# Performance work log

Measured on AMD Instinct MI355X. Metric: run time of the kernel, lower is better.

Reference implementation:

```python
import jax, jax.numpy as jnp
import numpy as np

N = 524288          # query points
N_COMP = 36         # sdf_n_comp
GRID = 512          # cubic grid resolution
SDF_DIM = 256
APP_DIM = 128
MAT_MODE = [(0, 1), (0, 2), (1, 2)]
VEC_MODE = [2, 1, 0]
PE_FREQS = (1.0, 2.0, 4.0)  # sdf_multires=3, log-sampled 2^0..2^2


def _pos_enc(x):
    # NeRF embedder, include_input=True: [x, sin(f x), cos(f x) per freq]
    outs = [x]
    for f in PE_FREQS:
        outs.append(jnp.sin(x * f))
        outs.append(jnp.cos(x * f))
    return jnp.concatenate(outs, axis=-1)  # (N, 21)


def _bilinear_plane(plane, gx, gy):
    # plane: (C, H, W); gx indexes W, gy indexes H; align_corners=True
    C, H, W = plane.shape
    px = (gx + 1.0) * 0.5 * (W - 1)
    py = (gy + 1.0) * 0.5 * (H - 1)
    x0 = jnp.clip(jnp.floor(px), 0, W - 2).astype(jnp.int32)
    y0 = jnp.clip(jnp.floor(py), 0, H - 2).astype(jnp.int32)
    x1, y1 = x0 + 1, y0 + 1
    wx = px - x0
    wy = py - y0
    f00 = plane[:, y0, x0]  # (C, N)
    f01 = plane[:, y0, x1]
    f10 = plane[:, y1, x0]
    f11 = plane[:, y1, x1]
    return (f00 * (1 - wx) + f01 * wx) * (1 - wy) + (f10 * (1 - wx) + f11 * wx) * wy


def _linear_line(line, g):
    # line: (C, L); g in [-1, 1]; align_corners=True
    C, L = line.shape
    p = (g + 1.0) * 0.5 * (L - 1)
    i0 = jnp.clip(jnp.floor(p), 0, L - 2).astype(jnp.int32)
    w = p - i0
    return line[:, i0] * (1 - w) + line[:, i0 + 1] * w  # (C, N)


def setup_inputs() -> dict:
    key = jax.random.key(0)
    ks = jax.random.split(key, 6)
    xyz = jax.random.uniform(ks[0], (N, 3), dtype=jnp.float32)  # points in aabb [0,1]^3
    planes = jax.random.normal(ks[1], (3, N_COMP, GRID, GRID), dtype=jnp.float32) * 0.1
    lines = jax.random.normal(ks[2], (3, N_COMP, GRID), dtype=jnp.float32) * 0.1
    in_ch = N_COMP * 3 + 21  # 129
    W1 = jax.random.normal(ks[3], (in_ch, SDF_DIM), dtype=jnp.float32) * (np.sqrt(2.0) / np.sqrt(SDF_DIM))
    b1 = jnp.zeros((SDF_DIM,), dtype=jnp.float32)
    W2 = jax.random.normal(ks[4], (SDF_DIM, 1 + APP_DIM), dtype=jnp.float32) * 0.0001 + np.sqrt(np.pi) / np.sqrt(SDF_DIM)
    b2 = jnp.full((1 + APP_DIM,), -0.2, dtype=jnp.float32)  # init_radius bias
    return {"xyz": xyz, "planes": planes, "lines": lines, "W1": W1, "b1": b1, "W2": W2, "b2": b2}


def reference(xyz, planes, lines, W1, b1, W2, b2):
    # contraction: normalize aabb [0,1]^3 -> [-1,1]
    xn = 2.0 * xyz - 1.0  # (N, 3)
    # sampling coords are detached in the original (coordinate_plane.detach())
    xs = jax.lax.stop_gradient(xn)
    feats = []
    for i in range(3):
        m0, m1 = MAT_MODE[i]
        pfeat = _bilinear_plane(planes[i], xs[:, m0], xs[:, m1])  # (C, N)
        lfeat = _linear_line(lines[i], xs[:, VEC_MODE[i]])        # (C, N)
        feats.append(pfeat * lfeat)
    feat = jnp.concatenate(feats, axis=0).T  # (N, 3C)
    pe = _pos_enc(xn)                         # (N, 21)
    h = jnp.concatenate([feat, pe], axis=-1)  # (N, 129)
    h = jax.nn.softplus(100.0 * (h @ W1 + b1)) / 100.0  # Softplus(beta=100)
    out = h @ W2 + b2  # (N, 1 + app_dim); out[..., :1] is the SDF
    return out
```

## Files before the change

### kernel.cpp

```cpp
#include <hip/hip_runtime.h>
#include <math.h>

typedef unsigned short u16;
typedef unsigned int u32;
typedef __attribute__((ext_vector_type(2))) u32 u32x2;
typedef __attribute__((ext_vector_type(8))) short short8;
typedef __attribute__((ext_vector_type(4))) float f32x4;

#define OFF_LINES_T 62914560u
#define OFF_W1S     63037440u
#define OFF_W2S     63119360u
#define WS_NEEDED   63217664u

__device__ __forceinline__ float bf_lo(u32 u){ union{u32 i;float f;} v; v.i = u << 16; return v.f; }
__device__ __forceinline__ float bf_hi(u32 u){ union{u32 i;float f;} v; v.i = u & 0xffff0000u; return v.f; }
__device__ __forceinline__ u16 f2bf(float f){ union{float f;u32 i;} v; v.f=f; u32 i=v.i; return (u16)((i + 0x7fffu + ((i>>16)&1u)) >> 16); }
__device__ __forceinline__ u32 pack2bf(float lo, float hi){ return (u32)f2bf(lo) | ((u32)f2bf(hi)<<16); }
__device__ __forceinline__ u32 pack2bf_fast(float lo, float hi){
  return __builtin_amdgcn_perm(__float_as_uint(hi) + 0x8000u,
                               __float_as_uint(lo) + 0x8000u, 0x07060302u);
}
__device__ __forceinline__ u16 f2bf_fast(float f){ return (u16)((__float_as_uint(f) + 0x8000u) >> 16); }

__global__ void k_tp(const float* __restrict__ planes, u16* __restrict__ pt){
  int t = blockIdx.x*256 + threadIdx.x;
  int i = t >> 18;
  int yx = t & 262143;
  const float* src = planes + (size_t)i*9437184 + yx;
  uint4* dst = reinterpret_cast<uint4*>(pt + (size_t)t*40);
#pragma unroll
  for (int cc=0; cc<5; cc++){
    float v[8];
#pragma unroll
    for (int e=0;e<8;e++){
      int c = cc*8+e;
      v[e] = (c<36) ? src[(size_t)c*262144] : 0.f;
    }
    uint4 o; o.x=pack2bf(v[0],v[1]); o.y=pack2bf(v[2],v[3]); o.z=pack2bf(v[4],v[5]); o.w=pack2bf(v[6],v[7]);
    dst[cc]=o;
  }
}

__global__ void k_tl(const float* __restrict__ lines, u16* __restrict__ lt){
  int t = blockIdx.x*256 + threadIdx.x;
  int i = t >> 9, g = t & 511;
  const float* src = lines + (size_t)i*18432 + g;
  uint4* dst = reinterpret_cast<uint4*>(lt + (size_t)t*40);
#pragma unroll
  for (int cc=0; cc<5; cc++){
    float v[8];
#pragma unroll
    for (int e=0;e<8;e++){
      int c = cc*8+e;
      v[e] = (c<36) ? src[(size_t)c*512] : 0.f;
    }
    uint4 o; o.x=pack2bf(v[0],v[1]); o.y=pack2bf(v[2],v[3]); o.z=pack2bf(v[4],v[5]); o.w=pack2bf(v[6],v[7]);
    dst[cc]=o;
  }
}

__device__ __forceinline__ int map_k1(int kp){
  if (kp < 120){ int g = kp/40, r = kp - g*40; return (r<36) ? g*36 + r : -1; }
  if (kp < 141) return kp - 12;
  return -1;
}

__global__ void k_w1(const float* __restrict__ W1, u16* __restrict__ w1s){
  int t = blockIdx.x*256 + threadIdx.x;
  int lane = t & 63;
  int fid = t >> 6;
  int nt = fid/5, kt = fid - nt*5;
  int n = nt*16 + (lane & 15);
  int kb = kt*32 + (lane >> 4)*8;
  float v[8];
#pragma unroll
  for (int j=0;j<8;j++){ int k = map_k1(kb+j); v[j] = (k>=0) ? W1[k*256+n] : 0.f; }
  uint4 o; o.x=pack2bf(v[0],v[1]); o.y=pack2bf(v[2],v[3]); o.z=pack2bf(v[4],v[5]); o.w=pack2bf(v[6],v[7]);
  *reinterpret_cast<uint4*>(w1s + (size_t)t*8) = o;
}

__global__ void k_w2(const float* __restrict__ W2, u16* __restrict__ w2s){
  int t = blockIdx.x*256 + threadIdx.x;
  int lane = t & 63;
  int fid = t >> 6;
  int kb = (fid & 7)*32 + (lane >> 4)*8;
  int n = (fid >> 3)*16 + (lane & 15);
  float v[8];
#pragma unroll
  for (int j=0;j<8;j++){ int k = kb+j; v[j] = (n<129) ? W2[k*129+n] : 0.f; }
  uint4 o; o.x=pack2bf(v[0],v[1]); o.y=pack2bf(v[2],v[3]); o.z=pack2bf(v[4],v[5]); o.w=pack2bf(v[6],v[7]);
  *reinterpret_cast<uint4*>(w2s + (size_t)t*8) = o;
}

__device__ __forceinline__ u32 blend(u32 u00,u32 u01,u32 u10,u32 u11,u32 g0,u32 g1,
                                     float wx,float wy,float wz){
  float r[2];
#pragma unroll
  for (int h=0; h<2; h++){
    float f00 = h ? bf_hi(u00) : bf_lo(u00);
    float f01 = h ? bf_hi(u01) : bf_lo(u01);
    float f10 = h ? bf_hi(u10) : bf_lo(u10);
    float f11 = h ? bf_hi(u11) : bf_lo(u11);
    float e0  = h ? bf_hi(g0)  : bf_lo(g0);
    float e1  = h ? bf_hi(g1)  : bf_lo(g1);
    float a  = f00 + (f01-f00)*wx;
    float b  = f10 + (f11-f10)*wx;
    float pf = a + (b-a)*wy;
    float lf = e0 + (e1-e0)*wz;
    r[h] = pf*lf;
  }
  return pack2bf_fast(r[0], r[1]);
}

#define FSTRIDE 168
#define HSTRIDE 264

__global__ void __launch_bounds__(512, 4) k_main(
    const float* __restrict__ xyz, const u16* __restrict__ pt,
    const u16* __restrict__ lt, const u16* __restrict__ w1s,
    const u16* __restrict__ w2s, const float* __restrict__ b1,
    const float* __restrict__ b2, float* __restrict__ out)
{
  __shared__ u16 smem[64*HSTRIDE];
  const int tid = threadIdx.x;
  const int p = tid >> 3, q = tid & 7;
  const int gp = blockIdx.x*64 + p;
  const float u0 = xyz[gp*3], u1 = xyz[gp*3+1], u2 = xyz[gp*3+2];
  const float xn0 = 2.f*u0-1.f, xn1 = 2.f*u1-1.f, xn2 = 2.f*u2-1.f;

  if (q < 6){
    const int i = q >> 1, part = q & 1;
    float gxv, gyv, gzv;
    if      (i==0){ gxv=xn0; gyv=xn1; gzv=xn2; }
    else if (i==1){ gxv=xn0; gyv=xn2; gzv=xn1; }
    else          { gxv=xn1; gyv=xn2; gzv=xn0; }
    float px=(gxv+1.0f)*0.5f*511.0f, py=(gyv+1.0f)*0.5f*511.0f, pz=(gzv+1.0f)*0.5f*511.0f;
    float fx=fminf(fmaxf(floorf(px),0.f),510.f);
    float fy=fminf(fmaxf(floorf(py),0.f),510.f);
    float fz=fminf(fmaxf(floorf(pz),0.f),510.f);
    int ix=(int)fx, iy=(int)fy, iz=(int)fz;
    float wx=px-fx, wy=py-fy, wz=pz-fz;
    const u16* base  = pt + (size_t)((i<<18)+(iy<<9)+ix)*40 + part*20;
    const u16* lbase = lt + (size_t)((i<<9)+iz)*40 + part*20;
    u16* dst = smem + p*FSTRIDE + i*40 + part*20;
#pragma unroll
    for (int c=0; c<5; c++){
      u32x2 a00 = *reinterpret_cast<const u32x2*>(base + c*4);
      u32x2 a01 = *reinterpret_cast<const u32x2*>(base + 40 + c*4);
      u32x2 a10 = *reinterpret_cast<const u32x2*>(base + 20480 + c*4);
      u32x2 a11 = *reinterpret_cast<const u32x2*>(base + 20520 + c*4);
      u32x2 e0  = *reinterpret_cast<const u32x2*>(lbase + c*4);
      u32x2 e1  = *reinterpret_cast<const u32x2*>(lbase + 40 + c*4);
      u32x2 o;
      o.x = blend(a00.x,a01.x,a10.x,a11.x,e0.x,e1.x,wx,wy,wz);
      o.y = blend(a00.y,a01.y,a10.y,a11.y,e0.y,e1.y,wx,wy,wz);
      *reinterpret_cast<u32x2*>(dst + c*4) = o;
    }
  } else if (q == 6){
    float v[21];
    v[0]=xn0; v[1]=xn1; v[2]=xn2;
    v[3]=__sinf(xn0);      v[4]=__sinf(xn1);      v[5]=__sinf(xn2);
    v[6]=__cosf(xn0);      v[7]=__cosf(xn1);      v[8]=__cosf(xn2);
    v[9]=__sinf(2.f*xn0);  v[10]=__sinf(2.f*xn1); v[11]=__sinf(2.f*xn2);
    v[12]=__cosf(2.f*xn0); v[13]=__cosf(2.f*xn1); v[14]=__cosf(2.f*xn2);
    v[15]=__sinf(4.f*xn0); v[16]=__sinf(4.f*xn1); v[17]=__sinf(4.f*xn2);
    v[18]=__cosf(4.f*xn0); v[19]=__cosf(4.f*xn1); v[20]=__cosf(4.f*xn2);
    u16* dst = smem + p*FSTRIDE + 120;
#pragma unroll
    for (int c=0; c<20; c++){
      float a = (c*2  <21)?v[c*2  ]:0.f;
      float b = (c*2+1<21)?v[c*2+1]:0.f;
      *reinterpret_cast<u32*>(dst + c*2) = pack2bf_fast(a,b);
    }
  }
  __syncthreads();

  const int lane = tid & 63;
  const int w = tid >> 6;
  const int wm = w & 1, wn = w >> 1;
  const int lm = lane & 15;
  const int quad = lane >> 4;
  const f32x4 zero = {0.f,0.f,0.f,0.f};
  f32x4 acc1[2][4];
#pragma unroll
  for (int mt=0; mt<2; mt++)
#pragma unroll
    for (int nt=0; nt<4; nt++) acc1[mt][nt] = zero;

#pragma unroll
  for (int kt=0; kt<5; kt++){
    short8 a[2];
#pragma unroll
    for (int mt=0; mt<2; mt++)
      a[mt] = *reinterpret_cast<const short8*>(smem + ((wm*2+mt)*16 + lm)*FSTRIDE + kt*32 + quad*8);
    short8 b[4];
#pragma unroll
    for (int nt=0; nt<4; nt++)
      b[nt] = *reinterpret_cast<const short8*>(w1s + (size_t)(((wn*4+nt)*5 + kt)*64 + lane)*8);
#pragma unroll
    for (int mt=0; mt<2; mt++)
#pragma unroll
      for (int nt=0; nt<4; nt++)
        acc1[mt][nt] = __builtin_amdgcn_mfma_f32_16x16x32_bf16(a[mt], b[nt], acc1[mt][nt], 0,0,0);
  }
  __syncthreads();

#pragma unroll
  for (int nt=0; nt<4; nt++){
    int col = wn*64 + nt*16 + lm;
    float bias = b1[col];
#pragma unroll
    for (int mt=0; mt<2; mt++){
#pragma unroll
      for (int r=0; r<4; r++){
        float xv = acc1[mt][nt][r] + bias;
        float z = 100.f*xv;
        float y = (z > 15.f) ? xv : __logf(1.f + __expf(z))*0.01f;
        int row = (wm*2+mt)*16 + quad*4 + r;
        smem[row*HSTRIDE + col] = f2bf_fast(y);
      }
    }
  }
  __syncthreads();

  f32x4 acc2[2][3];
#pragma unroll
  for (int mt=0; mt<2; mt++)
#pragma unroll
    for (int nt=0; nt<3; nt++) acc2[mt][nt] = zero;

#pragma unroll
  for (int kt=0; kt<8; kt++){
    short8 a[2];
#pragma unroll
    for (int mt=0; mt<2; mt++)
      a[mt] = *reinterpret_cast<const short8*>(smem + ((wm*2+mt)*16 + lm)*HSTRIDE + kt*32 + quad*8);
    short8 b[3];
#pragma unroll
    for (int nt=0; nt<3; nt++){
      int ntg = wn*3 + nt;
      b[nt] = *reinterpret_cast<const short8*>(w2s + (size_t)((ntg*8 + kt)*64 + lane)*8);
    }
#pragma unroll
    for (int mt=0; mt<2; mt++)
#pragma unroll
      for (int nt=0; nt<3; nt++)
        acc2[mt][nt] = __builtin_amdgcn_mfma_f32_16x16x32_bf16(a[mt], b[nt], acc2[mt][nt], 0,0,0);
  }

#pragma unroll
  for (int nt=0; nt<3; nt++){
    int j = (wn*3 + nt)*16 + lm;
    if (j < 129){
      float bias = b2[j];
#pragma unroll
      for (int mt=0; mt<2; mt++){
#pragma unroll
        for (int r=0; r<4; r++){
          int row = (wm*2+mt)*16 + quad*4 + r;
          out[(size_t)(blockIdx.x*64 + row)*129 + j] = acc2[mt][nt][r] + bias;
        }
      }
    }
  }
}

extern "C" void kernel_launch(void* const* d_in, const int* in_sizes, int n_in,
                              void* d_out, int out_size, void* d_ws, size_t ws_size,
                              hipStream_t stream) {
  const float* xyz    = (const float*)d_in[0];
  const float* planes = (const float*)d_in[1];
  const float* lines  = (const float*)d_in[2];
  const float* W1     = (const float*)d_in[3];
  const float* b1     = (const float*)d_in[4];
  const float* W2     = (const float*)d_in[5];
  const float* b2     = (const float*)d_in[6];
  if (ws_size < (size_t)WS_NEEDED) return;

  u16* pt  = (u16*)((char*)d_ws);
  u16* lt  = (u16*)((char*)d_ws + OFF_LINES_T);
  u16* w1s = (u16*)((char*)d_ws + OFF_W1S);
  u16* w2s = (u16*)((char*)d_ws + OFF_W2S);

  k_tp<<<3072, 256, 0, stream>>>(planes, pt);
  k_tl<<<6,    256, 0, stream>>>(lines,  lt);
  k_w1<<<20,   256, 0, stream>>>(W1, w1s);
  k_w2<<<24,   256, 0, stream>>>(W2, w2s);
  k_main<<<8192, 512, 0, stream>>>(xyz, pt, lt, w1s, w2s, b1, b2, (float*)d_out);
}
```

Baseline: 657.9 us.

## Merge preprocessing kernels, batch gather loads, packed blend, balance PE work, nontemporal stores

Measured after the change: 673.1 us. +2.3%, slower.

```diff
diff --git a/kernel.cpp b/kernel.cpp
--- a/kernel.cpp
+++ b/kernel.cpp
@@ -6,6 +6,7 @@
 typedef __attribute__((ext_vector_type(2))) u32 u32x2;
 typedef __attribute__((ext_vector_type(8))) short short8;
 typedef __attribute__((ext_vector_type(4))) float f32x4;
+typedef __attribute__((ext_vector_type(2))) float f32x2;
 
 #define OFF_LINES_T 62914560u
 #define OFF_W1S     63037440u
@@ -22,94 +23,95 @@
 }
 __device__ __forceinline__ u16 f2bf_fast(float f){ return (u16)((__float_as_uint(f) + 0x8000u) >> 16); }
 
-__global__ void k_tp(const float* __restrict__ planes, u16* __restrict__ pt){
-  int t = blockIdx.x*256 + threadIdx.x;
-  int i = t >> 18;
-  int yx = t & 262143;
-  const float* src = planes + (size_t)i*9437184 + yx;
-  uint4* dst = reinterpret_cast<uint4*>(pt + (size_t)t*40);
-#pragma unroll
-  for (int cc=0; cc<5; cc++){
-    float v[8];
-#pragma unroll
-    for (int e=0;e<8;e++){
-      int c = cc*8+e;
-      v[e] = (c<36) ? src[(size_t)c*262144] : 0.f;
-    }
-    uint4 o; o.x=pack2bf(v[0],v[1]); o.y=pack2bf(v[2],v[3]); o.z=pack2bf(v[4],v[5]); o.w=pack2bf(v[6],v[7]);
-    dst[cc]=o;
-  }
-}
-
-__global__ void k_tl(const float* __restrict__ lines, u16* __restrict__ lt){
-  int t = blockIdx.x*256 + threadIdx.x;
-  int i = t >> 9, g = t & 511;
-  const float* src = lines + (size_t)i*18432 + g;
-  uint4* dst = reinterpret_cast<uint4*>(lt + (size_t)t*40);
-#pragma unroll
-  for (int cc=0; cc<5; cc++){
-    float v[8];
-#pragma unroll
-    for (int e=0;e<8;e++){
-      int c = cc*8+e;
-      v[e] = (c<36) ? src[(size_t)c*512] : 0.f;
-    }
-    uint4 o; o.x=pack2bf(v[0],v[1]); o.y=pack2bf(v[2],v[3]); o.z=pack2bf(v[4],v[5]); o.w=pack2bf(v[6],v[7]);
-    dst[cc]=o;
-  }
-}
-
 __device__ __forceinline__ int map_k1(int kp){
   if (kp < 120){ int g = kp/40, r = kp - g*40; return (r<36) ? g*36 + r : -1; }
   if (kp < 141) return kp - 12;
   return -1;
 }
 
-__global__ void k_w1(const float* __restrict__ W1, u16* __restrict__ w1s){
-  int t = blockIdx.x*256 + threadIdx.x;
-  int lane = t & 63;
-  int fid = t >> 6;
-  int nt = fid/5, kt = fid - nt*5;
-  int n = nt*16 + (lane & 15);
-  int kb = kt*32 + (lane >> 4)*8;
-  float v[8];
-#pragma unroll
-  for (int j=0;j<8;j++){ int k = map_k1(kb+j); v[j] = (k>=0) ? W1[k*256+n] : 0.f; }
-  uint4 o; o.x=pack2bf(v[0],v[1]); o.y=pack2bf(v[2],v[3]); o.z=pack2bf(v[4],v[5]); o.w=pack2bf(v[6],v[7]);
-  *reinterpret_cast<uint4*>(w1s + (size_t)t*8) = o;
-}
-
-__global__ void k_w2(const float* __restrict__ W2, u16* __restrict__ w2s){
-  int t = blockIdx.x*256 + threadIdx.x;
-  int lane = t & 63;
-  int fid = t >> 6;
-  int kb = (fid & 7)*32 + (lane >> 4)*8;
-  int n = (fid >> 3)*16 + (lane & 15);
-  float v[8];
-#pragma unroll
-  for (int j=0;j<8;j++){ int k = kb+j; v[j] = (n<129) ? W2[k*129+n] : 0.f; }
-  uint4 o; o.x=pack2bf(v[0],v[1]); o.y=pack2bf(v[2],v[3]); o.z=pack2bf(v[4],v[5]); o.w=pack2bf(v[6],v[7]);
-  *reinterpret_cast<uint4*>(w2s + (size_t)t*8) = o;
-}
-
-__device__ __forceinline__ u32 blend(u32 u00,u32 u01,u32 u10,u32 u11,u32 g0,u32 g1,
-                                     float wx,float wy,float wz){
-  float r[2];
-#pragma unroll
-  for (int h=0; h<2; h++){
-    float f00 = h ? bf_hi(u00) : bf_lo(u00);
-    float f01 = h ? bf_hi(u01) : bf_lo(u01);
-    float f10 = h ? bf_hi(u10) : bf_lo(u10);
-    float f11 = h ? bf_hi(u11) : bf_lo(u11);
-    float e0  = h ? bf_hi(g0)  : bf_lo(g0);
-    float e1  = h ? bf_hi(g1)  : bf_lo(g1);
-    float a  = f00 + (f01-f00)*wx;
-    float b  = f10 + (f11-f10)*wx;
-    float pf = a + (b-a)*wy;
-    float lf = e0 + (e1-e0)*wz;
-    r[h] = pf*lf;
-  }
-  return pack2bf_fast(r[0], r[1]);
+#define NB_TP 3072
+#define NB_TL 6
+#define NB_W1 20
+#define NB_W2 24
+__global__ void k_pre(const float* __restrict__ planes, const float* __restrict__ lines,
+                      const float* __restrict__ W1, const float* __restrict__ W2,
+                      u16* __restrict__ pt, u16* __restrict__ lt,
+                      u16* __restrict__ w1s, u16* __restrict__ w2s){
+  const int b = blockIdx.x;
+  const int tid = threadIdx.x;
+  if (b < NB_TP){
+    int t = b*256 + tid;
+    int i = t >> 18;
+    int yx = t & 262143;
+    const float* src = planes + (size_t)i*9437184 + yx;
+    uint4* dst = reinterpret_cast<uint4*>(pt + (size_t)t*40);
+#pragma unroll
+    for (int cc=0; cc<5; cc++){
+      float v[8];
+#pragma unroll
+      for (int e=0;e<8;e++){
+        int c = cc*8+e;
+        v[e] = (c<36) ? src[(size_t)c*262144] : 0.f;
+      }
+      uint4 o; o.x=pack2bf(v[0],v[1]); o.y=pack2bf(v[2],v[3]); o.z=pack2bf(v[4],v[5]); o.w=pack2bf(v[6],v[7]);
+      dst[cc]=o;
+    }
+  } else if (b < NB_TP+NB_TL){
+    int t = (b-NB_TP)*256 + tid;
+    int i = t >> 9, g = t & 511;
+    const float* src = lines + (size_t)i*18432 + g;
+    uint4* dst = reinterpret_cast<uint4*>(lt + (size_t)t*40);
+#pragma unroll
+    for (int cc=0; cc<5; cc++){
+      float v[8];
+#pragma unroll
+      for (int e=0;e<8;e++){
+        int c = cc*8+e;
+        v[e] = (c<36) ? src[(size_t)c*512] : 0.f;
+      }
+      uint4 o; o.x=pack2bf(v[0],v[1]); o.y=pack2bf(v[2],v[3]); o.z=pack2bf(v[4],v[5]); o.w=pack2bf(v[6],v[7]);
+      dst[cc]=o;
+    }
+  } else if (b < NB_TP+NB_TL+NB_W1){
+    int t = (b-(NB_TP+NB_TL))*256 + tid;
+    int lane = t & 63;
+    int fid = t >> 6;
+    int nt = fid/5, kt = fid - nt*5;
+    int n = nt*16 + (lane & 15);
+    int kb = kt*32 + (lane >> 4)*8;
+    float v[8];
+#pragma unroll
+    for (int j=0;j<8;j++){ int k = map_k1(kb+j); v[j] = (k>=0) ? W1[k*256+n] : 0.f; }
+    uint4 o; o.x=pack2bf(v[0],v[1]); o.y=pack2bf(v[2],v[3]); o.z=pack2bf(v[4],v[5]); o.w=pack2bf(v[6],v[7]);
+    *reinterpret_cast<uint4*>(w1s + (size_t)t*8) = o;
+  } else {
+    int t = (b-(NB_TP+NB_TL+NB_W1))*256 + tid;
+    int lane = t & 63;
+    int fid = t >> 6;
+    int kb = (fid & 7)*32 + (lane >> 4)*8;
+    int n = (fid >> 3)*16 + (lane & 15);
+    float v[8];
+#pragma unroll
+    for (int j=0;j<8;j++){ int k = kb+j; v[j] = (n<129) ? W2[k*129+n] : 0.f; }
+    uint4 o; o.x=pack2bf(v[0],v[1]); o.y=pack2bf(v[2],v[3]); o.z=pack2bf(v[4],v[5]); o.w=pack2bf(v[6],v[7]);
+    *reinterpret_cast<uint4*>(w2s + (size_t)t*8) = o;
+  }
+}
+
+__device__ __forceinline__ f32x2 bfx2(u32 u){
+  f32x2 r;
+  r.x = __uint_as_float(u << 16);
+  r.y = __uint_as_float(u & 0xffff0000u);
+  return r;
+}
+
+__device__ __forceinline__ u32 blend2(u32 u00,u32 u01,u32 u10,u32 u11,u32 g0,u32 g1,
+                                      float w00,float w01,float w10,float w11,
+                                      float v0,float v1){
+  f32x2 pf = bfx2(u00)*w00 + bfx2(u01)*w01 + bfx2(u10)*w10 + bfx2(u11)*w11;
+  f32x2 lf = bfx2(g0)*v0 + bfx2(g1)*v1;
+  f32x2 r  = pf*lf;
+  return pack2bf_fast(r.x, r.y);
 }
 
 #define FSTRIDE 168
@@ -140,38 +142,49 @@
     float fz=fminf(fmaxf(floorf(pz),0.f),510.f);
     int ix=(int)fx, iy=(int)fy, iz=(int)fz;
     float wx=px-fx, wy=py-fy, wz=pz-fz;
+    const float cwx = 1.f-wx, cwy = 1.f-wy;
+    const float w00 = cwx*cwy, w01 = wx*cwy, w10 = cwx*wy, w11 = wx*wy;
+    const float v0 = 1.f-wz, v1 = wz;
     const u16* base  = pt + (size_t)((i<<18)+(iy<<9)+ix)*40 + part*20;
     const u16* lbase = lt + (size_t)((i<<9)+iz)*40 + part*20;
+
+    u32x2 A00[5],A01[5],A10[5],A11[5],E0[5],E1[5];
+#pragma unroll
+    for (int c=0; c<5; c++){
+      A00[c] = *reinterpret_cast<const u32x2*>(base + c*4);
+      A01[c] = *reinterpret_cast<const u32x2*>(base + 40 + c*4);
+      A10[c] = *reinterpret_cast<const u32x2*>(base + 20480 + c*4);
+      A11[c] = *reinterpret_cast<const u32x2*>(base + 20520 + c*4);
+      E0[c]  = *reinterpret_cast<const u32x2*>(lbase + c*4);
+      E1[c]  = *reinterpret_cast<const u32x2*>(lbase + 40 + c*4);
+    }
     u16* dst = smem + p*FSTRIDE + i*40 + part*20;
 #pragma unroll
     for (int c=0; c<5; c++){
-      u32x2 a00 = *reinterpret_cast<const u32x2*>(base + c*4);
-      u32x2 a01 = *reinterpret_cast<const u32x2*>(base + 40 + c*4);
-      u32x2 a10 = *reinterpret_cast<const u32x2*>(base + 20480 + c*4);
-      u32x2 a11 = *reinterpret_cast<const u32x2*>(base + 20520 + c*4);
-      u32x2 e0  = *reinterpret_cast<const u32x2*>(lbase + c*4);
-      u32x2 e1  = *reinterpret_cast<const u32x2*>(lbase + 40 + c*4);
       u32x2 o;
-      o.x = blend(a00.x,a01.x,a10.x,a11.x,e0.x,e1.x,wx,wy,wz);
-      o.y = blend(a00.y,a01.y,a10.y,a11.y,e0.y,e1.y,wx,wy,wz);
+      o.x = blend2(A00[c].x,A01[c].x,A10[c].x,A11[c].x,E0[c].x,E1[c].x, w00,w01,w10,w11,v0,v1);
+      o.y = blend2(A00[c].y,A01[c].y,A10[c].y,A11[c].y,E0[c].y,E1[c].y, w00,w01,w10,w11,v0,v1);
       *reinterpret_cast<u32x2*>(dst + c*4) = o;
     }
   } else if (q == 6){
-    float v[21];
+    float v[20];
     v[0]=xn0; v[1]=xn1; v[2]=xn2;
     v[3]=__sinf(xn0);      v[4]=__sinf(xn1);      v[5]=__sinf(xn2);
     v[6]=__cosf(xn0);      v[7]=__cosf(xn1);      v[8]=__cosf(xn2);
     v[9]=__sinf(2.f*xn0);  v[10]=__sinf(2.f*xn1); v[11]=__sinf(2.f*xn2);
     v[12]=__cosf(2.f*xn0); v[13]=__cosf(2.f*xn1); v[14]=__cosf(2.f*xn2);
     v[15]=__sinf(4.f*xn0); v[16]=__sinf(4.f*xn1); v[17]=__sinf(4.f*xn2);
-    v[18]=__cosf(4.f*xn0); v[19]=__cosf(4.f*xn1); v[20]=__cosf(4.f*xn2);
+    v[18]=__cosf(4.f*xn0); v[19]=__cosf(4.f*xn1);
     u16* dst = smem + p*FSTRIDE + 120;
 #pragma unroll
-    for (int c=0; c<20; c++){
-      float a = (c*2  <21)?v[c*2  ]:0.f;
-      float b = (c*2+1<21)?v[c*2+1]:0.f;
-      *reinterpret_cast<u32*>(dst + c*2) = pack2bf_fast(a,b);
-    }
+    for (int c=0; c<10; c++)
+      *reinterpret_cast<u32*>(dst + c*2) = pack2bf_fast(v[c*2], v[c*2+1]);
+  } else {
+    u16* dst = smem + p*FSTRIDE + 140;
+    *reinterpret_cast<u32*>(dst) = pack2bf_fast(__cosf(4.f*xn2), 0.f);
+#pragma unroll
+    for (int c=1; c<10; c++)
+      *reinterpret_cast<u32*>(dst + c*2) = 0u;
   }
   __syncthreads();
 
@@ -258,7 +271,8 @@
 #pragma unroll
         for (int r=0; r<4; r++){
           int row = (wm*2+mt)*16 + quad*4 + r;
-          out[(size_t)(blockIdx.x*64 + row)*129 + j] = acc2[mt][nt][r] + bias;
+          __builtin_nontemporal_store(acc2[mt][nt][r] + bias,
+                                      &out[(size_t)(blockIdx.x*64 + row)*129 + j]);
         }
       }
     }
@@ -282,9 +296,6 @@
   u16* w1s = (u16*)((char*)d_ws + OFF_W1S);
   u16* w2s = (u16*)((char*)d_ws + OFF_W2S);
 
-  k_tp<<<3072, 256, 0, stream>>>(planes, pt);
-  k_tl<<<6,    256, 0, stream>>>(lines,  lt);
-  k_w1<<<20,   256, 0, stream>>>(W1, w1s);
-  k_w2<<<24,   256, 0, stream>>>(W2, w2s);
+  k_pre<<<NB_TP+NB_TL+NB_W1+NB_W2, 256, 0, stream>>>(planes, lines, W1, W2, pt, lt, w1s, w2s);
   k_main<<<8192, 512, 0, stream>>>(xyz, pt, lt, w1s, w2s, b1, b2, (float*)d_out);
 }
```
